# Performance work log

Measured on AMD Instinct MI355X. Metric: run time of the kernel, lower is better.

Reference implementation:

```python
import jax, jax.numpy as jnp
import numpy as np

XBITS = 8  # bitconfig['xbits']


def quantize(x, bits=XBITS):
    """Per-tensor dynamic fixed-point fake-quant.
    topk(|x|, k=len, largest=False).max() == max(|x|), so the 'percentile' is a no-op.
    scale = 2**(bits - ceil(log2(max|x|)) - 1); clamp(round(x*scale), -t, t)/scale.
    """
    thresh = float(2 ** (bits - 1) - 1)
    max_abs = jnp.max(jnp.abs(x))
    # get_scale returns 0 on log2 domain error (threshold <= 0)
    exp = jnp.where(max_abs > 0, jnp.ceil(jnp.log2(max_abs)), jnp.zeros((), x.dtype))
    scale = jnp.exp2(jnp.asarray(bits, x.dtype) - exp - 1)
    return jnp.clip(jnp.round(x * scale), -thresh, thresh) / scale


def setup_inputs() -> dict:
    key = jax.random.key(0)
    k1, k2, k3 = jax.random.split(key, 3)
    N, D_in, D_out = 65536, 1024, 1024
    x = jax.random.normal(k1, (N, D_in), dtype=jnp.float32)
    weight = jax.random.normal(k2, (D_out, D_in), dtype=jnp.float32) * (1.0 / np.sqrt(D_in))
    bias = jax.random.normal(k3, (D_out,), dtype=jnp.float32) * (1.0 / np.sqrt(D_in))
    return {"x": x, "weight": weight, "bias": bias}


def reference(x, weight, bias):
    # FixedLinearFunction.forward: quantize both operands, matmul; bias is NOT added.
    q_x = quantize(x)
    q_w = quantize(weight)
    return q_x @ q_w.T  # [N, D_out]
```

## Files before the change

kernel.cpp:

```cpp
#include <hip/hip_runtime.h>
#include <stdint.h>

typedef int v4i  __attribute__((ext_vector_type(4)));
typedef int v16i __attribute__((ext_vector_type(16)));

__device__ __forceinline__ void async_load16(const void* g, void* l) {
    auto gp = (const __attribute__((address_space(1))) unsigned int*)(uintptr_t)g;
    auto lp = (__attribute__((address_space(3))) unsigned int*)(unsigned int)(uintptr_t)l;
    __builtin_amdgcn_global_load_lds(gp, lp, 16, 0, 0);
}

__global__ void k_init(unsigned* bits) {
    if (threadIdx.x < 2) bits[threadIdx.x] = 0u;
}

__global__ void k_absmax2(const float4* __restrict__ x, int nx4,
                          const float4* __restrict__ w, int nw4,
                          unsigned* __restrict__ bits) {
    const int XB = 2048;
    const float4* in; int n4, b, nb; unsigned* ob;
    if (blockIdx.x < XB) { in = x; n4 = nx4; b = blockIdx.x;      nb = XB;              ob = bits;     }
    else                 { in = w; n4 = nw4; b = blockIdx.x - XB; nb = gridDim.x - XB;  ob = bits + 1; }
    float m = 0.0f;
    int stride = nb * blockDim.x;
    for (int i = b * blockDim.x + threadIdx.x; i < n4; i += stride) {
        float4 v = in[i];
        m = fmaxf(m, fmaxf(fmaxf(fabsf(v.x), fabsf(v.y)),
                           fmaxf(fabsf(v.z), fabsf(v.w))));
    }
    #pragma unroll
    for (int off = 32; off > 0; off >>= 1)
        m = fmaxf(m, __shfl_down(m, off, 64));
    __shared__ float red[4];
    int lane = threadIdx.x & 63, wv = threadIdx.x >> 6;
    if (lane == 0) red[wv] = m;
    __syncthreads();
    if (threadIdx.x == 0) {
        m = fmaxf(fmaxf(red[0], red[1]), fmaxf(red[2], red[3]));
        atomicMax(ob, __float_as_uint(m));
    }
}

__global__ void k_scales(const unsigned* __restrict__ bits, float* __restrict__ sc) {
    float s[2];
    for (int i = 0; i < 2; ++i) {
        float m = __uint_as_float(bits[i]);
        int ex = 0;
        if (m > 0.0f) {
            int e;
            float f = frexpf(m, &e);
            ex = (f == 0.5f) ? (e - 1) : e;
        }
        s[i] = ldexpf(1.0f, 7 - ex);
    }
    sc[0] = s[0];
    sc[1] = s[1];
    sc[2] = 1.0f / (s[0] * s[1]);
}

__global__ void k_quant2(const float4* __restrict__ x, int* __restrict__ qx, int nx4,
                         const float4* __restrict__ w, int* __restrict__ qw, int nw4,
                         const float* __restrict__ scp) {
    const int XB = 4096;
    const float4* in; int* out; int n4, b, nb; float s;
    if (blockIdx.x < XB) { in = x; out = qx; n4 = nx4; b = blockIdx.x;      nb = XB;             s = scp[0]; }
    else                 { in = w; out = qw; n4 = nw4; b = blockIdx.x - XB; nb = gridDim.x - XB; s = scp[1]; }
    int stride = nb * blockDim.x;
    for (int i = b * blockDim.x + threadIdx.x; i < n4; i += stride) {
        float4 v = in[i];
        int qa = (int)rintf(v.x * s); qa = qa > 127 ? 127 : (qa < -127 ? -127 : qa);
        int qb = (int)rintf(v.y * s); qb = qb > 127 ? 127 : (qb < -127 ? -127 : qb);
        int qc = (int)rintf(v.z * s); qc = qc > 127 ? 127 : (qc < -127 ? -127 : qc);
        int qd = (int)rintf(v.w * s); qd = qd > 127 ? 127 : (qd < -127 ? -127 : qd);
        out[i] = (qa & 0xff) | ((qb & 0xff) << 8) | ((qc & 0xff) << 16) | (qd << 24);
    }
}

__global__ __launch_bounds__(256) void k_gemm(const signed char* __restrict__ A,
                                              const signed char* __restrict__ B,
                                              float* __restrict__ out,
                                              const float* __restrict__ scp) {
    __shared__ __align__(16) signed char As[128 * 128];
    __shared__ __align__(16) signed char Bs[128 * 128];
    const int tid  = threadIdx.x;
    const int lane = tid & 63;
    const int wave = tid >> 6;
    const int wm   = wave & 1;
    const int wn   = wave >> 1;
    const int l31  = lane & 31;
    const int lhi  = lane >> 5;

    const int orig = blockIdx.x;
    const int v    = (orig & 7) * 512 + (orig >> 3);
    const int n0   = (v & 7) * 128;
    const int m0   = (v >> 3) * 128;

    v16i acc[2][2];
    #pragma unroll
    for (int a = 0; a < 2; ++a)
        #pragma unroll
        for (int b = 0; b < 2; ++b)
            #pragma unroll
            for (int i = 0; i < 16; ++i) acc[a][b][i] = 0;

    const signed char* gAsrc[4];
    const signed char* gBsrc[4];
    #pragma unroll
    for (int s = 0; s < 4; ++s) {
        int i  = s * 256 + tid;
        int p  = i >> 3;
        int qs = (i & 7) ^ (p & 7);
        gAsrc[s] = A + (size_t)(m0 + p) * 1024 + qs * 16;
        gBsrc[s] = B + (size_t)(n0 + p) * 1024 + qs * 16;
    }
    signed char* lA = As + tid * 16;
    signed char* lB = Bs + tid * 16;

    const int rA = wm * 64 + l31;
    const int rB = wn * 64 + l31;
    const signed char* pA0 = As + rA * 128;
    const signed char* pB0 = Bs + rB * 128;
    const int xA = rA & 7;
    const int xB = rB & 7;

    for (int k0 = 0; k0 < 1024; k0 += 128) {
        #pragma unroll
        for (int s = 0; s < 4; ++s) {
            async_load16(gAsrc[s] + k0, lA + s * 4096);
            async_load16(gBsrc[s] + k0, lB + s * 4096);
        }
        __syncthreads();
        #pragma unroll
        for (int kc = 0; kc < 4; ++kc) {
            const int c  = kc * 2 + lhi;
            const int qa = (c ^ xA) * 16;
            const int qb = (c ^ xB) * 16;
            v4i a0 = *(const v4i*)(pA0 + qa);
            v4i a1 = *(const v4i*)(pA0 + 32 * 128 + qa);
            v4i b0 = *(const v4i*)(pB0 + qb);
            v4i b1 = *(const v4i*)(pB0 + 32 * 128 + qb);
            acc[0][0] = __builtin_amdgcn_mfma_i32_32x32x32_i8(a0, b0, acc[0][0], 0, 0, 0);
            acc[0][1] = __builtin_amdgcn_mfma_i32_32x32x32_i8(a0, b1, acc[0][1], 0, 0, 0);
            acc[1][0] = __builtin_amdgcn_mfma_i32_32x32x32_i8(a1, b0, acc[1][0], 0, 0, 0);
            acc[1][1] = __builtin_amdgcn_mfma_i32_32x32x32_i8(a1, b1, acc[1][1], 0, 0, 0);
        }
        __syncthreads();
    }

    const float inv = scp[0];
    #pragma unroll
    for (int tm = 0; tm < 2; ++tm)
        #pragma unroll
        for (int tn = 0; tn < 2; ++tn)
            #pragma unroll
            for (int r = 0; r < 16; ++r) {
                int row = m0 + wm * 64 + tm * 32 + (r & 3) + 8 * (r >> 2) + 4 * lhi;
                int col = n0 + wn * 64 + tn * 32 + l31;
                out[(size_t)row * 1024 + col] = (float)acc[tm][tn][r] * inv;
            }
}

extern "C" void kernel_launch(void* const* d_in, const int* in_sizes, int n_in,
                              void* d_out, int out_size, void* d_ws, size_t ws_size,
                              hipStream_t stream) {
    const float* x = (const float*)d_in[0];
    const float* w = (const float*)d_in[1];
    float* out = (float*)d_out;

    const int NX = 65536 * 1024;
    const int NW = 1024 * 1024;

    char* ws = (char*)d_ws;
    unsigned* bits = (unsigned*)ws;
    float* sc = (float*)(ws + 8);
    signed char* qx = (signed char*)(ws + 256);
    signed char* qw = qx + (size_t)NX;

    k_init<<<1, 64, 0, stream>>>(bits);
    k_absmax2<<<2048 + 128, 256, 0, stream>>>((const float4*)x, NX / 4,
                                              (const float4*)w, NW / 4, bits);
    k_scales<<<1, 1, 0, stream>>>(bits, sc);
    k_quant2<<<4096 + 128, 256, 0, stream>>>((const float4*)x, (int*)qx, NX / 4,
                                             (const float4*)w, (int*)qw, NW / 4, sc);

    k_gemm<<<dim3(4096), 256, 0, stream>>>(qx, qw, out, sc + 2);
}
```

Measured before the change: 586.0 us.

## Enlarge int8 GEMM tile to 256x256 with double-buffered async LDS pipeline

Reworks the int8 MFMA GEMM to use 256x256 output tiles per 512-thread block, with eight waves each computing a 128x64 subtile. K is staged in 64-wide slices into two LDS buffers, so global-to-LDS loads for later slices overlap with the MFMA work on the current one, synchronised by vmcnt waits and raw barriers. The larger tile raises operand reuse and cuts global traffic for A and B. The cost is more accumulator registers and 64KB of LDS per block, which limits occupancy. The XOR swizzle is changed to match the 64-byte row layout.

```diff
diff --git a/kernel.cpp b/kernel.cpp
--- a/kernel.cpp
+++ b/kernel.cpp
@@ -76,85 +76,101 @@
     }
 }
 
-__global__ __launch_bounds__(256) void k_gemm(const signed char* __restrict__ A,
-                                              const signed char* __restrict__ B,
-                                              float* __restrict__ out,
-                                              const float* __restrict__ scp) {
-    __shared__ __align__(16) signed char As[128 * 128];
-    __shared__ __align__(16) signed char Bs[128 * 128];
+#define GBAR()  __builtin_amdgcn_s_barrier()
+#define WAITV4() asm volatile("s_waitcnt vmcnt(4)" ::: "memory")
+#define WAITV0() asm volatile("s_waitcnt vmcnt(0)" ::: "memory")
+
+__global__ __launch_bounds__(512, 2) void k_gemm(const signed char* __restrict__ A,
+                                                 const signed char* __restrict__ B,
+                                                 float* __restrict__ out,
+                                                 const float* __restrict__ scp) {
+    __shared__ __align__(16) signed char lds[4 * 16384];
     const int tid  = threadIdx.x;
     const int lane = tid & 63;
     const int wave = tid >> 6;
-    const int wm   = wave & 1;
-    const int wn   = wave >> 1;
+    const int wm   = wave >> 2;
+    const int wn   = wave & 3;
     const int l31  = lane & 31;
     const int lhi  = lane >> 5;
 
     const int orig = blockIdx.x;
-    const int v    = (orig & 7) * 512 + (orig >> 3);
-    const int n0   = (v & 7) * 128;
-    const int m0   = (v >> 3) * 128;
-
-    v16i acc[2][2];
-    #pragma unroll
-    for (int a = 0; a < 2; ++a)
+    const int v    = (orig & 7) * 128 + (orig >> 3);
+    const int n0   = (v & 3) * 256;
+    const int m0   = (v >> 2) * 256;
+
+    v16i acc[4][2];
+    #pragma unroll
+    for (int a = 0; a < 4; ++a)
         #pragma unroll
         for (int b = 0; b < 2; ++b)
             #pragma unroll
             for (int i = 0; i < 16; ++i) acc[a][b][i] = 0;
 
-    const signed char* gAsrc[4];
-    const signed char* gBsrc[4];
-    #pragma unroll
-    for (int s = 0; s < 4; ++s) {
-        int i  = s * 256 + tid;
-        int p  = i >> 3;
-        int qs = (i & 7) ^ (p & 7);
-        gAsrc[s] = A + (size_t)(m0 + p) * 1024 + qs * 16;
-        gBsrc[s] = B + (size_t)(n0 + p) * 1024 + qs * 16;
-    }
-    signed char* lA = As + tid * 16;
-    signed char* lB = Bs + tid * 16;
-
-    const int rA = wm * 64 + l31;
-    const int rB = wn * 64 + l31;
-    const signed char* pA0 = As + rA * 128;
-    const signed char* pB0 = Bs + rB * 128;
-    const int xA = rA & 7;
-    const int xB = rB & 7;
-
-    for (int k0 = 0; k0 < 1024; k0 += 128) {
-        #pragma unroll
-        for (int s = 0; s < 4; ++s) {
-            async_load16(gAsrc[s] + k0, lA + s * 4096);
-            async_load16(gBsrc[s] + k0, lB + s * 4096);
+    const signed char* gA[2];
+    const signed char* gB[2];
+    #pragma unroll
+    for (int s = 0; s < 2; ++s) {
+        int i = s * 512 + tid;
+        int p = i >> 2;
+        int q = (i & 3) ^ ((p >> 1) & 3);
+        gA[s] = A + (size_t)(m0 + p) * 1024 + q * 16;
+        gB[s] = B + (size_t)(n0 + p) * 1024 + q * 16;
+    }
+
+    auto STAGE = [&](int cur, int k0) {
+        signed char* base = lds + cur * 32768;
+        #pragma unroll
+        for (int s = 0; s < 2; ++s) {
+            async_load16(gA[s] + k0, base +         s * 8192 + tid * 16);
+            async_load16(gB[s] + k0, base + 16384 + s * 8192 + tid * 16);
         }
-        __syncthreads();
-        #pragma unroll
-        for (int kc = 0; kc < 4; ++kc) {
-            const int c  = kc * 2 + lhi;
-            const int qa = (c ^ xA) * 16;
-            const int qb = (c ^ xB) * 16;
-            v4i a0 = *(const v4i*)(pA0 + qa);
-            v4i a1 = *(const v4i*)(pA0 + 32 * 128 + qa);
-            v4i b0 = *(const v4i*)(pB0 + qb);
-            v4i b1 = *(const v4i*)(pB0 + 32 * 128 + qb);
-            acc[0][0] = __builtin_amdgcn_mfma_i32_32x32x32_i8(a0, b0, acc[0][0], 0, 0, 0);
-            acc[0][1] = __builtin_amdgcn_mfma_i32_32x32x32_i8(a0, b1, acc[0][1], 0, 0, 0);
-            acc[1][0] = __builtin_amdgcn_mfma_i32_32x32x32_i8(a1, b0, acc[1][0], 0, 0, 0);
-            acc[1][1] = __builtin_amdgcn_mfma_i32_32x32x32_i8(a1, b1, acc[1][1], 0, 0, 0);
+    };
+
+    const int key = (l31 >> 1) & 3;
+    auto COMPUTE = [&](int cur) {
+        const signed char* Ab = lds + cur * 32768;
+        const signed char* Bb = Ab + 16384;
+        #pragma unroll
+        for (int ks = 0; ks < 2; ++ks) {
+            const int slot = ((ks * 2 + lhi) ^ key) * 16;
+            v4i af[4], bf[2];
+            #pragma unroll
+            for (int tm = 0; tm < 4; ++tm)
+                af[tm] = *(const v4i*)(Ab + (wm * 128 + tm * 32 + l31) * 64 + slot);
+            #pragma unroll
+            for (int tn = 0; tn < 2; ++tn)
+                bf[tn] = *(const v4i*)(Bb + (wn * 64 + tn * 32 + l31) * 64 + slot);
+            #pragma unroll
+            for (int tm = 0; tm < 4; ++tm)
+                #pragma unroll
+                for (int tn = 0; tn < 2; ++tn)
+                    acc[tm][tn] = __builtin_amdgcn_mfma_i32_32x32x32_i8(
+                        af[tm], bf[tn], acc[tm][tn], 0, 0, 0);
         }
-        __syncthreads();
-    }
+    };
+
+    STAGE(0, 0);
+    STAGE(1, 64);
+
+    #pragma unroll 2
+    for (int t = 0; t < 14; ++t) {
+        WAITV4();
+        GBAR();
+        COMPUTE(t & 1);
+        GBAR();
+        STAGE(t & 1, (t + 2) * 64);
+    }
+    WAITV4(); GBAR(); COMPUTE(0); GBAR();
+    WAITV0(); GBAR(); COMPUTE(1);
 
     const float inv = scp[0];
     #pragma unroll
-    for (int tm = 0; tm < 2; ++tm)
+    for (int tm = 0; tm < 4; ++tm)
         #pragma unroll
         for (int tn = 0; tn < 2; ++tn)
             #pragma unroll
             for (int r = 0; r < 16; ++r) {
-                int row = m0 + wm * 64 + tm * 32 + (r & 3) + 8 * (r >> 2) + 4 * lhi;
+                int row = m0 + wm * 128 + tm * 32 + (r & 3) + 8 * (r >> 2) + 4 * lhi;
                 int col = n0 + wn * 64 + tn * 32 + l31;
                 out[(size_t)row * 1024 + col] = (float)acc[tm][tn][r] * inv;
             }
@@ -183,5 +199,5 @@
     k_quant2<<<4096 + 128, 256, 0, stream>>>((const float4*)x, (int*)qx, NX / 4,
                                              (const float4*)w, (int*)qw, NW / 4, sc);
 
-    k_gemm<<<dim3(4096), 256, 0, stream>>>(qx, qw, out, sc + 2);
-}
+    k_gemm<<<dim3(1024), 512, 0, stream>>>(qx, qw, out, sc + 2);
+}
```

After: 587.8 us. Within noise of the previous version (+0.3%).
